# Performance work log

Hardware: AMD Instinct MI355X
Metric: run time of the kernel (lower is better)

The kernel has to match this reference:

```python
import jax, jax.numpy as jnp
import numpy as np

N_NODES = 50000
N_EDGES = 800000
IN_DIM = 1200   # latent_size * num_heads
OUT_DIM = 300
NEG_SLOPE = 0.2  # PyG GATConv default


def setup_inputs() -> dict:
    key = jax.random.key(0)
    k1, k2, k3, k4, k5 = jax.random.split(key, 5)
    z = jax.random.normal(k1, (N_NODES, IN_DIM), dtype=jnp.float32)
    edge_index = jax.random.randint(k2, (2, N_EDGES), 0, N_NODES, dtype=jnp.int64)
    # GATConv params (heads=1): lin weight [out, in], attention vectors [out], bias [out]
    W = jax.random.normal(k3, (OUT_DIM, IN_DIM), dtype=jnp.float32) * (1.0 / np.sqrt(IN_DIM))
    att_src = jax.random.normal(k4, (OUT_DIM,), dtype=jnp.float32) * 0.1
    att_dst = jax.random.normal(k5, (OUT_DIM,), dtype=jnp.float32) * 0.1
    bias = jnp.zeros((OUT_DIM,), dtype=jnp.float32)
    return {"z": z, "edge_index": edge_index, "W": W,
            "att_src": att_src, "att_dst": att_dst, "bias": bias}


def reference(z, edge_index, W, att_src, att_dst, bias):
    N = z.shape[0]
    # Linear projection (no bias on lin in GATConv; bias added after aggregation)
    x = z @ W.T                                   # [N, OUT_DIM]
    # add self-loops (GATConv default add_self_loops=True)
    loop = jnp.arange(N, dtype=edge_index.dtype)
    src = jnp.concatenate([edge_index[0], loop])  # message source j
    dst = jnp.concatenate([edge_index[1], loop])  # message target i
    # per-node attention logits
    a_src = x @ att_src                           # [N]
    a_dst = x @ att_dst                           # [N]
    # per-edge score, softmax over incoming edges of each target node
    e = jax.nn.leaky_relu(a_src[src] + a_dst[dst], negative_slope=NEG_SLOPE)  # [E+N]
    e_max = jax.ops.segment_max(e, dst, num_segments=N)   # every node has a self-loop
    ex = jnp.exp(e - e_max[dst])
    denom = jax.ops.segment_sum(ex, dst, num_segments=N)
    alpha = ex / denom[dst]                       # [E+N]
    # weighted aggregation (scatter-add over targets)
    out = jax.ops.segment_sum(alpha[:, None] * x[src], dst, num_segments=N)
    return out + bias
```

## Files before the change

### kernel.cpp

```cpp
#include <hip/hip_runtime.h>

#define N_NODES 50000
#define N_EDGES 800000
#define IN_DIM  1200
#define KP      1216
#define OUT_DIM 300
#define BNP     320
#define XBS     304
#define BM      64
#define NKT     38
#define GRID_M  ((N_NODES + BM - 1) / BM)

typedef __attribute__((ext_vector_type(8))) short short8;
typedef __attribute__((ext_vector_type(4))) float f32x4;

__device__ __forceinline__ short f2bf(float f) {
  unsigned u = __builtin_bit_cast(unsigned, f);
  u += 0x7fffu + ((u >> 16) & 1u);
  return (short)(u >> 16);
}
__device__ __forceinline__ float bf2f(unsigned short h) {
  return __builtin_bit_cast(float, (unsigned)h << 16);
}
__device__ __forceinline__ float lrelu(float v) { return v > 0.f ? v : 0.2f * v; }

__device__ __forceinline__ float wredMaxF(float v) {
  #pragma unroll
  for (int o = 32; o > 0; o >>= 1) v = fmaxf(v, __shfl_xor(v, o));
  return v;
}
__device__ __forceinline__ float wredSumF(float v) {
  #pragma unroll
  for (int o = 32; o > 0; o >>= 1) v += __shfl_xor(v, o);
  return v;
}

__device__ __forceinline__ void gl_lds16(const unsigned short* g, unsigned short* l) {
  __builtin_amdgcn_global_load_lds(
      (const __attribute__((address_space(1))) unsigned int*)g,
      (__attribute__((address_space(3))) unsigned int*)l, 16, 0, 0);
}

__global__ __launch_bounds__(256) void wconv(const float* __restrict__ W,
                                             unsigned short* __restrict__ Wb) {
  int f = blockIdx.x * 256 + threadIdx.x;
  if (f >= BNP * KP / 8) return;
  int n = (f * 8) / KP, c = (f * 8) % KP;
  short8 v = {0,0,0,0,0,0,0,0};
  if (n < OUT_DIM && c < IN_DIM) {
    const float4* p = reinterpret_cast<const float4*>(W + (size_t)n * IN_DIM + c);
    float4 f0 = p[0], f1 = p[1];
    v[0]=f2bf(f0.x); v[1]=f2bf(f0.y); v[2]=f2bf(f0.z); v[3]=f2bf(f0.w);
    v[4]=f2bf(f1.x); v[5]=f2bf(f1.y); v[6]=f2bf(f1.z); v[7]=f2bf(f1.w);
  }
  *reinterpret_cast<short8*>(&Wb[(size_t)n * KP + c]) = v;
}

__global__ __launch_bounds__(256) void gemm_x(const float* __restrict__ z,
                                              const unsigned short* __restrict__ Wb,
                                              const float* __restrict__ att_s,
                                              const float* __restrict__ att_d,
                                              unsigned short* __restrict__ xb,
                                              float* __restrict__ a_s,
                                              float* __restrict__ a_d) {
  __shared__ __align__(16) unsigned short As[2][BM * 32];
  __shared__ __align__(16) unsigned short Bs[2][BNP * 32];

  const int tid  = threadIdx.x;
  const int lane = tid & 63;
  const int wid  = tid >> 6;
  const int lr   = lane & 15;
  const int lg   = lane >> 4;
  const int mw   = wid >> 1;
  const int nw   = wid & 1;
  const int m0   = blockIdx.x * BM;

  f32x4 zero4 = {0.f, 0.f, 0.f, 0.f};
  const float4 fz4 = make_float4(0.f, 0.f, 0.f, 0.f);
  f32x4 acc[2][10];
  #pragma unroll
  for (int mf = 0; mf < 2; ++mf)
    #pragma unroll
    for (int nj = 0; nj < 10; ++nj) acc[mf][nj] = zero4;

  const int ra = tid >> 2, ka8 = (tid & 3) * 8;
  const int am = m0 + ra;
  float4 ga0, ga1;

  const int brow = wid * 16 + (lane >> 2);
  const int bk8  = (lane & 3) * 8;

  #define LOADA(KT)                                                           \
    {                                                                         \
      int k = (KT) * 32 + ka8;                                                \
      if (am < N_NODES && k + 8 <= IN_DIM) {                                  \
        const float4* p = reinterpret_cast<const float4*>(z + (size_t)am * IN_DIM + k); \
        ga0 = p[0]; ga1 = p[1];                                               \
      } else { ga0 = fz4; ga1 = fz4; }                                        \
    }

  #define WRITEA(BUF)                                                         \
    {                                                                         \
      short8 v;                                                               \
      v[0]=f2bf(ga0.x); v[1]=f2bf(ga0.y); v[2]=f2bf(ga0.z); v[3]=f2bf(ga0.w); \
      v[4]=f2bf(ga1.x); v[5]=f2bf(ga1.y); v[6]=f2bf(ga1.z); v[7]=f2bf(ga1.w); \
      *reinterpret_cast<short8*>(&As[BUF][ra * 32 + ka8]) = v;                \
    }

  #define STAGEB(BUF, KT)                                                     \
    _Pragma("unroll")                                                         \
    for (int j = 0; j < 5; ++j) {                                             \
      const unsigned short* gsrc =                                            \
          Wb + (size_t)(j * 64 + brow) * KP + (KT) * 32 + bk8;                \
      unsigned short* ldst = &Bs[BUF][(j * 64 + wid * 16) * 32];              \
      gl_lds16(gsrc, ldst);                                                   \
    }

  STAGEB(0, 0);
  LOADA(0);
  WRITEA(0);
  __syncthreads();

  #pragma unroll 1
  for (int kt = 0; kt < NKT; ++kt) {
    const int cur = kt & 1;
    if (kt < NKT - 1) {
      STAGEB(cur ^ 1, kt + 1);
      LOADA(kt + 1);
    }

    short8 a0 = *reinterpret_cast<const short8*>(&As[cur][(mw * 32 + lr) * 32 + lg * 8]);
    short8 a1 = *reinterpret_cast<const short8*>(&As[cur][(mw * 32 + 16 + lr) * 32 + lg * 8]);
    #pragma unroll
    for (int nj = 0; nj < 10; ++nj) {
      short8 b = *reinterpret_cast<const short8*>(
          &Bs[cur][(nw * 160 + nj * 16 + lr) * 32 + lg * 8]);
      acc[0][nj] = __builtin_amdgcn_mfma_f32_16x16x32_bf16(a0, b, acc[0][nj], 0, 0, 0);
      acc[1][nj] = __builtin_amdgcn_mfma_f32_16x16x32_bf16(a1, b, acc[1][nj], 0, 0, 0);
    }

    if (kt < NKT - 1) { WRITEA(cur ^ 1); }
    __syncthreads();
  }
  #undef LOADA
  #undef WRITEA
  #undef STAGEB

  float* red = reinterpret_cast<float*>(&As[0][0]);

  float ps[2][4] = {{0,0,0,0},{0,0,0,0}}, pd[2][4] = {{0,0,0,0},{0,0,0,0}};
  #pragma unroll
  for (int nj = 0; nj < 10; ++nj) {
    int c = nw * 160 + nj * 16 + lr;
    bool cv = c < OUT_DIM;
    float vs = cv ? att_s[c] : 0.f;
    float vd = cv ? att_d[c] : 0.f;
    #pragma unroll
    for (int mf = 0; mf < 2; ++mf) {
      #pragma unroll
      for (int jj = 0; jj < 4; ++jj) {
        float val = acc[mf][nj][jj];
        int r = m0 + mw * 32 + mf * 16 + 4 * lg + jj;
        if (cv && r < N_NODES) xb[(size_t)r * XBS + c] = (unsigned short)f2bf(val);
        ps[mf][jj] += val * vs;
        pd[mf][jj] += val * vd;
      }
    }
  }
  #pragma unroll
  for (int mf = 0; mf < 2; ++mf)
    #pragma unroll
    for (int jj = 0; jj < 4; ++jj) {
      #pragma unroll
      for (int o = 8; o > 0; o >>= 1) {
        ps[mf][jj] += __shfl_xor(ps[mf][jj], o);
        pd[mf][jj] += __shfl_xor(pd[mf][jj], o);
      }
      if (lr == 0) {
        int rr = mw * 32 + mf * 16 + 4 * lg + jj;
        red[nw * 64 + rr]       = ps[mf][jj];
        red[128 + nw * 64 + rr] = pd[mf][jj];
      }
    }
  __syncthreads();
  if (tid < 64) {
    int r = m0 + tid;
    if (r < N_NODES) a_s[r] = red[tid] + red[64 + tid];
  } else if (tid < 128) {
    int t = tid - 64, r = m0 + t;
    if (r < N_NODES) a_d[r] = red[128 + t] + red[192 + t];
  }
}

__global__ void hist(const int* __restrict__ ei, int* __restrict__ deg) {
  int e = blockIdx.x * blockDim.x + threadIdx.x;
  if (e < N_EDGES) {
    unsigned dst = (unsigned)ei[N_EDGES + e];
    if (dst < N_NODES) atomicAdd(&deg[dst], 1);
  }
}

#define SCAN_B 1024
#define NBLK   49

__global__ __launch_bounds__(SCAN_B) void scan1(const int* __restrict__ deg,
                                                int* __restrict__ bsum) {
  int i = blockIdx.x * SCAN_B + threadIdx.x;
  int v = (i < N_NODES) ? deg[i] : 0;
  #pragma unroll
  for (int o = 32; o > 0; o >>= 1) v += __shfl_xor(v, o);
  __shared__ int wt[16];
  if ((threadIdx.x & 63) == 0) wt[threadIdx.x >> 6] = v;
  __syncthreads();
  if (threadIdx.x == 0) {
    int t = 0;
    #pragma unroll
    for (int w = 0; w < 16; ++w) t += wt[w];
    bsum[blockIdx.x] = t;
  }
}

__global__ void scan2(const int* __restrict__ bsum, int* __restrict__ bex,
                      int* __restrict__ offs) {
  int l = threadIdx.x;
  int v = (l < NBLK) ? bsum[l] : 0;
  int incl = v;
  #pragma unroll
  for (int off = 1; off < 64; off <<= 1) {
    int u = __shfl_up(incl, off);
    if (l >= off) incl += u;
  }
  if (l < NBLK) bex[l] = incl - v;
  if (l == NBLK - 1) offs[N_NODES] = incl;
}

__global__ __launch_bounds__(SCAN_B) void scan3(const int* __restrict__ deg,
                                                const int* __restrict__ bex,
                                                int* __restrict__ offs,
                                                int* __restrict__ cursor) {
  int tid = threadIdx.x;
  int i = blockIdx.x * SCAN_B + tid;
  int lane = tid & 63, wid = tid >> 6;
  int v = (i < N_NODES) ? deg[i] : 0;
  int incl = v;
  #pragma unroll
  for (int off = 1; off < 64; off <<= 1) {
    int u = __shfl_up(incl, off);
    if (lane >= off) incl += u;
  }
  __shared__ int wt[16];
  if (lane == 63) wt[wid] = incl;
  __syncthreads();
  if (tid < 16) {
    int t = wt[tid];
    int sc = t;
    #pragma unroll
    for (int off = 1; off < 16; off <<= 1) {
      int u = __shfl_up(sc, off);
      if (tid >= off) sc += u;
    }
    wt[tid] = sc - t;
  }
  __syncthreads();
  int excl = incl - v + wt[wid] + bex[blockIdx.x];
  if (i < N_NODES) { offs[i] = excl; cursor[i] = excl; }
}

__global__ void fill(const int* __restrict__ ei, int* __restrict__ cursor,
                     int* __restrict__ srcs) {
  int e = blockIdx.x * blockDim.x + threadIdx.x;
  if (e < N_EDGES) {
    unsigned dst = (unsigned)ei[N_EDGES + e];
    unsigned src = (unsigned)ei[e];
    if (dst < N_NODES && src < N_NODES) {
      int pos = atomicAdd(&cursor[dst], 1);
      srcs[pos] = (int)src;
    }
  }
}

__global__ __launch_bounds__(256) void minv_k(const float* __restrict__ a_s,
                                              const float* __restrict__ a_d,
                                              const int* __restrict__ offs,
                                              const int* __restrict__ srcs,
                                              float2* __restrict__ minv) {
  int node = blockIdx.x * 4 + (threadIdx.x >> 6);
  if (node >= N_NODES) return;
  int lane = threadIdx.x & 63;
  int beg = offs[node], end = offs[node + 1];
  float adi = a_d[node];
  float eself = lrelu(a_s[node] + adi);

  float m = eself;
  for (int k = beg + lane; k < end; k += 64)
    m = fmaxf(m, lrelu(a_s[srcs[k]] + adi));
  m = wredMaxF(m);

  float s = 0.f;
  for (int k = beg + lane; k < end; k += 64)
    s += expf(lrelu(a_s[srcs[k]] + adi) - m);
  s = wredSumF(s) + expf(eself - m);
  if (lane == 0) minv[node] = make_float2(m, 1.0f / s);
}

#define CCH 15
__global__ __launch_bounds__(256) void aggregate(const unsigned short* __restrict__ xb,
                                                 const float* __restrict__ a_s,
                                                 const float* __restrict__ a_d,
                                                 const float2* __restrict__ minv,
                                                 const int* __restrict__ offs,
                                                 const int* __restrict__ srcs,
                                                 const float* __restrict__ bias,
                                                 float* __restrict__ out) {
  unsigned wi = blockIdx.x * 256u + threadIdx.x;
  if (wi >= (unsigned)N_NODES * CCH) return;
  unsigned node = wi / CCH;
  unsigned cc = wi - node * CCH;

  int beg = offs[node], end = offs[node + 1];
  float2 mi = minv[node];
  const float m = mi.x, inv = mi.y;
  const float adi = a_d[node];
  const float wself = expf(lrelu(a_s[node] + adi) - m) * inv;

  const unsigned short* xcol = xb + 20u * cc;

  float acc[20];
  {
    const unsigned short* xr = xcol + (size_t)node * XBS;
    #pragma unroll
    for (int q = 0; q < 5; ++q) {
      ushort4 xv = *reinterpret_cast<const ushort4*>(xr + 4 * q);
      acc[4*q+0] = wself * bf2f(xv.x);
      acc[4*q+1] = wself * bf2f(xv.y);
      acc[4*q+2] = wself * bf2f(xv.z);
      acc[4*q+3] = wself * bf2f(xv.w);
    }
  }

  for (int k = beg; k < end; ++k) {
    int sj = srcs[k];
    float w = expf(lrelu(a_s[sj] + adi) - m) * inv;
    const unsigned short* xr = xcol + (size_t)sj * XBS;
    #pragma unroll
    for (int q = 0; q < 5; ++q) {
      ushort4 xv = *reinterpret_cast<const ushort4*>(xr + 4 * q);
      acc[4*q+0] += w * bf2f(xv.x);
      acc[4*q+1] += w * bf2f(xv.y);
      acc[4*q+2] += w * bf2f(xv.z);
      acc[4*q+3] += w * bf2f(xv.w);
    }
  }
  float* op = out + (size_t)node * OUT_DIM + 20u * cc;
  const float* bp = bias + 20u * cc;
  #pragma unroll
  for (int q = 0; q < 5; ++q) {
    float4 b = *reinterpret_cast<const float4*>(bp + 4 * q);
    float4 o = {acc[4*q] + b.x, acc[4*q+1] + b.y, acc[4*q+2] + b.z, acc[4*q+3] + b.w};
    *reinterpret_cast<float4*>(op + 4 * q) = o;
  }
}

extern "C" void kernel_launch(void* const* d_in, const int* in_sizes, int n_in,
                              void* d_out, int out_size, void* d_ws, size_t ws_size,
                              hipStream_t stream) {
  const float* z     = (const float*)d_in[0];
  const int*   ei    = (const int*)d_in[1];
  const float* W     = (const float*)d_in[2];
  const float* att_s = (const float*)d_in[3];
  const float* att_d = (const float*)d_in[4];
  const float* bias  = (const float*)d_in[5];
  float* out = (float*)d_out;

  char* ws = (char*)d_ws;
  size_t off = 0;
  unsigned short* xb = (unsigned short*)(ws + off); off += (size_t)N_NODES * XBS * 2;
  unsigned short* Wb = (unsigned short*)(ws + off); off += (size_t)BNP * KP * 2;
  float*  a_s  = (float*)(ws + off);  off += 50048 * 4;
  float*  a_d  = (float*)(ws + off);  off += 50048 * 4;
  int*    deg  = (int*)(ws + off);    off += 50048 * 4;
  int*    offs = (int*)(ws + off);    off += 50056 * 4;
  int*    cur  = (int*)(ws + off);    off += 50048 * 4;
  int*    bsum = (int*)(ws + off);    off += 64 * 4;
  int*    bex  = (int*)(ws + off);    off += 64 * 4;
  int*    srcs = (int*)(ws + off);    off += (size_t)N_EDGES * 4;
  float2* minv = (float2*)(ws + off); off += (size_t)50048 * 8;

  (void)hipMemsetAsync(deg, 0, N_NODES * 4, stream);

  wconv<<<(BNP * KP / 8 + 255) / 256, 256, 0, stream>>>(W, Wb);
  gemm_x<<<GRID_M, 256, 0, stream>>>(z, Wb, att_s, att_d, xb, a_s, a_d);
  hist<<<(N_EDGES + 255) / 256, 256, 0, stream>>>(ei, deg);
  scan1<<<NBLK, SCAN_B, 0, stream>>>(deg, bsum);
  scan2<<<1, 64, 0, stream>>>(bsum, bex, offs);
  scan3<<<NBLK, SCAN_B, 0, stream>>>(deg, bex, offs, cur);
  fill<<<(N_EDGES + 255) / 256, 256, 0, stream>>>(ei, cur, srcs);
  minv_k<<<(N_NODES + 3) / 4, 256, 0, stream>>>(a_s, a_d, offs, srcs, minv);
  aggregate<<<((unsigned)N_NODES * CCH + 255) / 256, 256, 0, stream>>>(
      xb, a_s, a_d, minv, offs, srcs, bias, out);
}
```

Baseline: 329.4 us.

## Swizzle LDS tiles and reshape GEMM warp tiling to 64x80 per wave

Applies an XOR swizzle to the bf16 A and B tiles in shared memory, to cut bank conflicts on the short8 reads. For B the swizzle is done by permuting the global source address of the direct-to-LDS loads. Each wave now covers all 64 rows and an 80-column strip instead of a 32x160 quadrant. That lowers shared-memory reads per MFMA group from 12 to 9. The epilogue reduction of the attention logits is extended to sum four per-wave partials, at the cost of more live accumulator registers per wave.

```diff
diff --git a/kernel.cpp b/kernel.cpp
--- a/kernel.cpp
+++ b/kernel.cpp
@@ -71,28 +71,29 @@
   const int wid  = tid >> 6;
   const int lr   = lane & 15;
   const int lg   = lane >> 4;
-  const int mw   = wid >> 1;
-  const int nw   = wid & 1;
+  const int lrs  = (lr >> 1) & 3;
   const int m0   = blockIdx.x * BM;
 
   f32x4 zero4 = {0.f, 0.f, 0.f, 0.f};
   const float4 fz4 = make_float4(0.f, 0.f, 0.f, 0.f);
-  f32x4 acc[2][10];
-  #pragma unroll
-  for (int mf = 0; mf < 2; ++mf)
-    #pragma unroll
-    for (int nj = 0; nj < 10; ++nj) acc[mf][nj] = zero4;
-
-  const int ra = tid >> 2, ka8 = (tid & 3) * 8;
-  const int am = m0 + ra;
+  f32x4 acc[4][5];
+  #pragma unroll
+  for (int mf = 0; mf < 4; ++mf)
+    #pragma unroll
+    for (int nj = 0; nj < 5; ++nj) acc[mf][nj] = zero4;
+
+  const int ra  = tid >> 2;
+  const int kaL = tid & 3;
+  const int kaP = kaL ^ ((ra >> 1) & 3);
+  const int am  = m0 + ra;
   float4 ga0, ga1;
 
   const int brow = wid * 16 + (lane >> 2);
-  const int bk8  = (lane & 3) * 8;
+  const int bgc  = (lane & 3) ^ ((lane >> 3) & 3);
 
   #define LOADA(KT)                                                           \
     {                                                                         \
-      int k = (KT) * 32 + ka8;                                                \
+      int k = (KT) * 32 + kaL * 8;                                            \
       if (am < N_NODES && k + 8 <= IN_DIM) {                                  \
         const float4* p = reinterpret_cast<const float4*>(z + (size_t)am * IN_DIM + k); \
         ga0 = p[0]; ga1 = p[1];                                               \
@@ -104,14 +105,14 @@
       short8 v;                                                               \
       v[0]=f2bf(ga0.x); v[1]=f2bf(ga0.y); v[2]=f2bf(ga0.z); v[3]=f2bf(ga0.w); \
       v[4]=f2bf(ga1.x); v[5]=f2bf(ga1.y); v[6]=f2bf(ga1.z); v[7]=f2bf(ga1.w); \
-      *reinterpret_cast<short8*>(&As[BUF][ra * 32 + ka8]) = v;                \
+      *reinterpret_cast<short8*>(&As[BUF][ra * 32 + kaP * 8]) = v;            \
     }
 
   #define STAGEB(BUF, KT)                                                     \
     _Pragma("unroll")                                                         \
     for (int j = 0; j < 5; ++j) {                                             \
       const unsigned short* gsrc =                                            \
-          Wb + (size_t)(j * 64 + brow) * KP + (KT) * 32 + bk8;                \
+          Wb + (size_t)(j * 64 + brow) * KP + (KT) * 32 + bgc * 8;            \
       unsigned short* ldst = &Bs[BUF][(j * 64 + wid * 16) * 32];              \
       gl_lds16(gsrc, ldst);                                                   \
     }
@@ -129,14 +130,18 @@
       LOADA(kt + 1);
     }
 
-    short8 a0 = *reinterpret_cast<const short8*>(&As[cur][(mw * 32 + lr) * 32 + lg * 8]);
-    short8 a1 = *reinterpret_cast<const short8*>(&As[cur][(mw * 32 + 16 + lr) * 32 + lg * 8]);
-    #pragma unroll
-    for (int nj = 0; nj < 10; ++nj) {
+    short8 a[4];
+    #pragma unroll
+    for (int mf = 0; mf < 4; ++mf)
+      a[mf] = *reinterpret_cast<const short8*>(
+          &As[cur][(mf * 16 + lr) * 32 + (lg ^ lrs) * 8]);
+    #pragma unroll
+    for (int nj = 0; nj < 5; ++nj) {
       short8 b = *reinterpret_cast<const short8*>(
-          &Bs[cur][(nw * 160 + nj * 16 + lr) * 32 + lg * 8]);
-      acc[0][nj] = __builtin_amdgcn_mfma_f32_16x16x32_bf16(a0, b, acc[0][nj], 0, 0, 0);
-      acc[1][nj] = __builtin_amdgcn_mfma_f32_16x16x32_bf16(a1, b, acc[1][nj], 0, 0, 0);
+          &Bs[cur][(wid * 80 + nj * 16 + lr) * 32 + (lg ^ lrs) * 8]);
+      #pragma unroll
+      for (int mf = 0; mf < 4; ++mf)
+        acc[mf][nj] = __builtin_amdgcn_mfma_f32_16x16x32_bf16(a[mf], b, acc[mf][nj], 0, 0, 0);
     }
 
     if (kt < NKT - 1) { WRITEA(cur ^ 1); }
@@ -148,19 +153,24 @@
 
   float* red = reinterpret_cast<float*>(&As[0][0]);
 
-  float ps[2][4] = {{0,0,0,0},{0,0,0,0}}, pd[2][4] = {{0,0,0,0},{0,0,0,0}};
-  #pragma unroll
-  for (int nj = 0; nj < 10; ++nj) {
-    int c = nw * 160 + nj * 16 + lr;
+  float ps[4][4], pd[4][4];
+  #pragma unroll
+  for (int mf = 0; mf < 4; ++mf)
+    #pragma unroll
+    for (int jj = 0; jj < 4; ++jj) { ps[mf][jj] = 0.f; pd[mf][jj] = 0.f; }
+
+  #pragma unroll
+  for (int nj = 0; nj < 5; ++nj) {
+    int c = wid * 80 + nj * 16 + lr;
     bool cv = c < OUT_DIM;
     float vs = cv ? att_s[c] : 0.f;
     float vd = cv ? att_d[c] : 0.f;
     #pragma unroll
-    for (int mf = 0; mf < 2; ++mf) {
+    for (int mf = 0; mf < 4; ++mf) {
       #pragma unroll
       for (int jj = 0; jj < 4; ++jj) {
         float val = acc[mf][nj][jj];
-        int r = m0 + mw * 32 + mf * 16 + 4 * lg + jj;
+        int r = m0 + mf * 16 + 4 * lg + jj;
         if (cv && r < N_NODES) xb[(size_t)r * XBS + c] = (unsigned short)f2bf(val);
         ps[mf][jj] += val * vs;
         pd[mf][jj] += val * vd;
@@ -168,7 +178,7 @@
     }
   }
   #pragma unroll
-  for (int mf = 0; mf < 2; ++mf)
+  for (int mf = 0; mf < 4; ++mf)
     #pragma unroll
     for (int jj = 0; jj < 4; ++jj) {
       #pragma unroll
@@ -177,18 +187,20 @@
         pd[mf][jj] += __shfl_xor(pd[mf][jj], o);
       }
       if (lr == 0) {
-        int rr = mw * 32 + mf * 16 + 4 * lg + jj;
-        red[nw * 64 + rr]       = ps[mf][jj];
-        red[128 + nw * 64 + rr] = pd[mf][jj];
+        int rr = mf * 16 + 4 * lg + jj;
+        red[wid * 64 + rr]       = ps[mf][jj];
+        red[256 + wid * 64 + rr] = pd[mf][jj];
       }
     }
   __syncthreads();
   if (tid < 64) {
     int r = m0 + tid;
-    if (r < N_NODES) a_s[r] = red[tid] + red[64 + tid];
+    if (r < N_NODES)
+      a_s[r] = red[tid] + red[64 + tid] + red[128 + tid] + red[192 + tid];
   } else if (tid < 128) {
     int t = tid - 64, r = m0 + t;
-    if (r < N_NODES) a_d[r] = red[128 + t] + red[192 + t];
+    if (r < N_NODES)
+      a_d[r] = red[256 + t] + red[256 + 64 + t] + red[256 + 128 + t] + red[256 + 192 + t];
   }
 }
 
```

Result: no change. 329.3 us (-0.0%).

## Split GEMM N dimension across two blocks with XCD remap and LDS swizzle

Applied to the files above, without the earlier changes.

Splits each 64-row tile of the projection GEMM into two blocks, each covering 160 output columns, which doubles the grid and halves accumulator registers per thread. Block IDs are remapped so that neighbouring logical tiles, which share the same z rows, land on the same XCD for L2 reuse. An XOR swizzle is applied to the A and B LDS layouts to reduce bank conflicts. Because each block now produces only a partial attention-logit sum, the per-node a_s and a_d values are accumulated with atomicAdd after an extra memset. The cost is that the z tile is read and converted to bf16 twice.

```diff
diff --git a/kernel.cpp b/kernel.cpp
--- a/kernel.cpp
+++ b/kernel.cpp
@@ -10,6 +10,7 @@
 #define BM      64
 #define NKT     38
 #define GRID_M  ((N_NODES + BM - 1) / BM)
+#define GRID_G  (GRID_M * 2)
 
 typedef __attribute__((ext_vector_type(8))) short short8;
 typedef __attribute__((ext_vector_type(4))) float f32x4;
@@ -64,35 +65,43 @@
                                               float* __restrict__ a_s,
                                               float* __restrict__ a_d) {
   __shared__ __align__(16) unsigned short As[2][BM * 32];
-  __shared__ __align__(16) unsigned short Bs[2][BNP * 32];
+  __shared__ __align__(16) unsigned short Bs[2][160 * 32];
+
+  const int orig = blockIdx.x;
+  const int xcd  = orig & 7, rem = orig >> 3;
+  const int base = (xcd < 4) ? xcd * 196 : 784 + (xcd - 4) * 195;
+  const int logical = base + rem;
+  const int m0 = (logical >> 1) * BM;
+  const int n0 = (logical & 1) * 160;
 
   const int tid  = threadIdx.x;
   const int lane = tid & 63;
   const int wid  = tid >> 6;
   const int lr   = lane & 15;
   const int lg   = lane >> 4;
+  const int lrs  = (lr >> 1) & 3;
   const int mw   = wid >> 1;
   const int nw   = wid & 1;
-  const int m0   = blockIdx.x * BM;
 
   f32x4 zero4 = {0.f, 0.f, 0.f, 0.f};
   const float4 fz4 = make_float4(0.f, 0.f, 0.f, 0.f);
-  f32x4 acc[2][10];
+  f32x4 acc[2][5];
   #pragma unroll
   for (int mf = 0; mf < 2; ++mf)
     #pragma unroll
-    for (int nj = 0; nj < 10; ++nj) acc[mf][nj] = zero4;
-
-  const int ra = tid >> 2, ka8 = (tid & 3) * 8;
-  const int am = m0 + ra;
+    for (int nj = 0; nj < 5; ++nj) acc[mf][nj] = zero4;
+
+  const int ra  = tid >> 2;
+  const int kaL = tid & 3;
+  const int kaP = kaL ^ ((ra >> 1) & 3);
+  const int am  = m0 + ra;
   float4 ga0, ga1;
 
-  const int brow = wid * 16 + (lane >> 2);
-  const int bk8  = (lane & 3) * 8;
+  const int bgc = (lane & 3) ^ ((lane >> 3) & 3);
 
   #define LOADA(KT)                                                           \
     {                                                                         \
-      int k = (KT) * 32 + ka8;                                                \
+      int k = (KT) * 32 + kaL * 8;                                            \
       if (am < N_NODES && k + 8 <= IN_DIM) {                                  \
         const float4* p = reinterpret_cast<const float4*>(z + (size_t)am * IN_DIM + k); \
         ga0 = p[0]; ga1 = p[1];                                               \
@@ -104,16 +113,17 @@
       short8 v;                                                               \
       v[0]=f2bf(ga0.x); v[1]=f2bf(ga0.y); v[2]=f2bf(ga0.z); v[3]=f2bf(ga0.w); \
       v[4]=f2bf(ga1.x); v[5]=f2bf(ga1.y); v[6]=f2bf(ga1.z); v[7]=f2bf(ga1.w); \
-      *reinterpret_cast<short8*>(&As[BUF][ra * 32 + ka8]) = v;                \
+      *reinterpret_cast<short8*>(&As[BUF][ra * 32 + kaP * 8]) = v;            \
     }
 
   #define STAGEB(BUF, KT)                                                     \
     _Pragma("unroll")                                                         \
-    for (int j = 0; j < 5; ++j) {                                             \
-      const unsigned short* gsrc =                                            \
-          Wb + (size_t)(j * 64 + brow) * KP + (KT) * 32 + bk8;                \
-      unsigned short* ldst = &Bs[BUF][(j * 64 + wid * 16) * 32];              \
-      gl_lds16(gsrc, ldst);                                                   \
+    for (int j = 0; j < 10; ++j) {                                            \
+      if ((j & 3) == wid) {                                                   \
+        const unsigned short* gsrc =                                          \
+            Wb + (size_t)(n0 + j * 16 + (lane >> 2)) * KP + (KT) * 32 + bgc * 8; \
+        gl_lds16(gsrc, &Bs[BUF][j * 16 * 32]);                                \
+      }                                                                       \
     }
 
   STAGEB(0, 0);
@@ -129,12 +139,14 @@
       LOADA(kt + 1);
     }
 
-    short8 a0 = *reinterpret_cast<const short8*>(&As[cur][(mw * 32 + lr) * 32 + lg * 8]);
-    short8 a1 = *reinterpret_cast<const short8*>(&As[cur][(mw * 32 + 16 + lr) * 32 + lg * 8]);
-    #pragma unroll
-    for (int nj = 0; nj < 10; ++nj) {
+    short8 a0 = *reinterpret_cast<const short8*>(
+        &As[cur][(mw * 32 + lr) * 32 + (lg ^ lrs) * 8]);
+    short8 a1 = *reinterpret_cast<const short8*>(
+        &As[cur][(mw * 32 + 16 + lr) * 32 + (lg ^ lrs) * 8]);
+    #pragma unroll
+    for (int nj = 0; nj < 5; ++nj) {
       short8 b = *reinterpret_cast<const short8*>(
-          &Bs[cur][(nw * 160 + nj * 16 + lr) * 32 + lg * 8]);
+          &Bs[cur][(nw * 80 + nj * 16 + lr) * 32 + (lg ^ lrs) * 8]);
       acc[0][nj] = __builtin_amdgcn_mfma_f32_16x16x32_bf16(a0, b, acc[0][nj], 0, 0, 0);
       acc[1][nj] = __builtin_amdgcn_mfma_f32_16x16x32_bf16(a1, b, acc[1][nj], 0, 0, 0);
     }
@@ -150,8 +162,8 @@
 
   float ps[2][4] = {{0,0,0,0},{0,0,0,0}}, pd[2][4] = {{0,0,0,0},{0,0,0,0}};
   #pragma unroll
-  for (int nj = 0; nj < 10; ++nj) {
-    int c = nw * 160 + nj * 16 + lr;
+  for (int nj = 0; nj < 5; ++nj) {
+    int c = n0 + nw * 80 + nj * 16 + lr;
     bool cv = c < OUT_DIM;
     float vs = cv ? att_s[c] : 0.f;
     float vd = cv ? att_d[c] : 0.f;
@@ -185,10 +197,10 @@
   __syncthreads();
   if (tid < 64) {
     int r = m0 + tid;
-    if (r < N_NODES) a_s[r] = red[tid] + red[64 + tid];
+    if (r < N_NODES) atomicAdd(&a_s[r], red[tid] + red[64 + tid]);
   } else if (tid < 128) {
     int t = tid - 64, r = m0 + t;
-    if (r < N_NODES) a_d[r] = red[128 + t] + red[192 + t];
+    if (r < N_NODES) atomicAdd(&a_d[r], red[128 + t] + red[192 + t]);
   }
 }
 
@@ -387,9 +399,10 @@
   float2* minv = (float2*)(ws + off); off += (size_t)50048 * 8;
 
   (void)hipMemsetAsync(deg, 0, N_NODES * 4, stream);
+  (void)hipMemsetAsync(a_s, 0, 2 * 50048 * 4, stream);
 
   wconv<<<(BNP * KP / 8 + 255) / 256, 256, 0, stream>>>(W, Wb);
-  gemm_x<<<GRID_M, 256, 0, stream>>>(z, Wb, att_s, att_d, xb, a_s, a_d);
+  gemm_x<<<GRID_G, 256, 0, stream>>>(z, Wb, att_s, att_d, xb, a_s, a_d);
   hist<<<(N_EDGES + 255) / 256, 256, 0, stream>>>(ei, deg);
   scan1<<<NBLK, SCAN_B, 0, stream>>>(deg, bsum);
   scan2<<<1, 64, 0, stream>>>(bsum, bex, offs);
```

After: 358.2 us. 1.09x slower.
